# Kernel optimization log

Hardware: AMD Instinct MI355X
Metric: run time of the kernel (lower is better)

## Reference

```python
import jax, jax.numpy as jnp
import numpy as np

SAMPLE_RATE = 24000
THRESHOLD_FACTOR = 5.0
MAX_SPIKE_SAMPLES = int(0.0015 * SAMPLE_RATE)  # 36
K_MAX = 65536  # static upper bound on number of threshold crossings
N_SAMPLES = 24_000_000


def setup_inputs() -> dict:
    key = jax.random.key(0)
    x = jax.random.normal(key, (N_SAMPLES,), dtype=jnp.float32)
    return {"data_detected": x}


def _detect_one(v, threshold):
    """Detect peaks of v above +threshold. For the negative pass, call with -x
    (x < -thr  <=>  -x > thr, and argmin(x) == argmax(-x)). Returns an int32
    array of length K_MAX: valid peak indices first (sorted), padded with -1."""
    N = v.shape[0]
    mask = (v > threshold).astype(jnp.int32)
    d = jnp.diff(mask)  # +1 = entry (False->True), -1 = exit (True->False)
    entries = jnp.nonzero(d == 1, size=K_MAX, fill_value=N)[0]
    exits = jnp.nonzero(d == -1, size=K_MAX, fill_value=N)[0]
    n = jnp.minimum(jnp.sum(d == 1), jnp.sum(d == -1))
    idx = jnp.arange(K_MAX)
    dur = exits - entries
    keep = (idx < n) & (dur <= MAX_SPIKE_SAMPLES)
    # vectorized windowed peak search: (K_MAX, W) gather + row argmax
    win_idx = jnp.clip(entries[:, None] + jnp.arange(MAX_SPIKE_SAMPLES)[None, :], 0, N - 1)
    windows = v[win_idx]
    peaks = entries + jnp.argmax(windows, axis=1)
    # compact valid peaks to the front (entries are sorted), pad with -1
    peaks = jnp.sort(jnp.where(keep, peaks, N))
    total = jnp.sum(keep)
    return jnp.where(idx < total, peaks, -1)


def reference(data_detected):
    x = data_detected
    threshold = THRESHOLD_FACTOR * jnp.median(jnp.abs(x)) / 0.6745
    pos_indices = _detect_one(x, threshold)
    neg_indices = _detect_one(-x, threshold)
    return pos_indices, neg_indices, threshold
```

## Files before the change

### kernel.cpp

```cpp
#include <hip/hip_runtime.h>
#include <stdint.h>

#define HB 18
#define SH_SIZE 8192
#define NSAMP 65536
#define SMARG 1912
#define DBITS 22
#define CAND_CAP 8192
#define CSORT_CAP 4096
#define CBUF_CAP 256
#define LIST_CAP 2500000
#define LBUF_CAP 4096
#define PAIR_CAP 512
#define PEAK_CAP 512
#define MAX_SPIKE 36
#define AB_BLOCKS 128
#define TILE 2048

#define P_ULO   0
#define P_UHI   1
#define P_THRLO 2
#define P_THR   3
#define P_CANDN 4
#define P_LISTN 5
#define P_CB    6
#define P_BINA1 7
#define P_BINA2 8
#define P_RA1   9
#define P_RA2   10
#define P_DONES 11
#define P_DONEA 12
#define P_DONEB 13

#define WS_SHIST  0
#define WS_HISTA  32768
#define WS_HISTB  40960
#define WS_PARAMS 57344
#define WS_ZERO_BYTES 57408
#define WS_CAND   57600
#define WS_LIST   102400

__global__ __launch_bounds__(256) void k_prep(int* __restrict__ ws, int nInts,
                                              float* __restrict__ out, int n2) {
  int j = blockIdx.x * 256 + threadIdx.x;
  if (j < nInts) ws[j] = 0;
  if (j < n2) out[j] = -1.0f;
}

__global__ __launch_bounds__(256) void k_sample(const float* __restrict__ x, int N,
                                                int* __restrict__ shist,
                                                int* __restrict__ p) {
  __shared__ int h[SH_SIZE];
  __shared__ int lastS;
  __shared__ int part[256];
  __shared__ int excl[256];
  __shared__ uint32_t uLoS, uHiS;
  int tid = threadIdx.x;
  for (int i = tid; i < SH_SIZE; i += 256) h[i] = 0;
  __syncthreads();
  int stride = N / NSAMP; if (stride < 1) stride = 1;
  for (int i = blockIdx.x * 256 + tid; i < NSAMP; i += gridDim.x * 256) {
    long long idx = (long long)i * stride;
    if (idx < N) {
      uint32_t u = __float_as_uint(x[idx]) & 0x7fffffffu;
      atomicAdd(&h[u >> HB], 1);
    }
  }
  __syncthreads();
  for (int i = tid; i < SH_SIZE; i += 256) {
    int c = h[i];
    if (c) atomicAdd(&shist[i], c);
  }
  __threadfence();
  if (tid == 0) lastS = (atomicAdd(&p[P_DONES], 1) == (int)gridDim.x - 1);
  __syncthreads();
  if (!lastS) return;
  __threadfence();
  const int chunk = SH_SIZE / 256;
  int base = tid * chunk;
  int s = 0;
  int cc[chunk];
  for (int w = 0; w < chunk; ++w) { cc[w] = shist[base + w]; s += cc[w]; }
  part[tid] = s;
  __syncthreads();
  if (tid == 0) { int a = 0; for (int i = 0; i < 256; ++i) { excl[i] = a; a += part[i]; } }
  __syncthreads();
  int pre = excl[tid];
  int sA = NSAMP / 2 - SMARG, sB = NSAMP / 2 + SMARG;
  if (pre <= sA && sA < pre + s) {
    int a = pre;
    for (int w = 0; w < chunk; ++w) {
      if (sA < a + cc[w]) { uLoS = (uint32_t)(base + w) << HB; break; }
      a += cc[w];
    }
  }
  if (pre <= sB && sB < pre + s) {
    int a = pre;
    for (int w = 0; w < chunk; ++w) {
      if (sB < a + cc[w]) { uHiS = (uint32_t)(base + w + 1) << HB; break; }
      a += cc[w];
    }
  }
  __syncthreads();
  if (tid == 0) {
    uint32_t uLo = uLoS, uHi = uHiS;
    if (uHi - uLo > (1u << DBITS)) uHi = uLo + (1u << DBITS);
    p[P_ULO] = (int)uLo;
    p[P_UHI] = (int)uHi;
    float vLo = __uint_as_float(uLo);
    p[P_THRLO] = __float_as_int((5.0f * vLo / 0.6745f) * 0.999f);
  }
}

__device__ inline void m_elem(uint32_t fbits, int idx, uint32_t uLo, uint32_t bw,
                              uint32_t thrBits, int* lbuf, int* lcnt,
                              int* cbuf, int* ccnt, int& cb) {
  uint32_t u = fbits & 0x7fffffffu;
  cb += (u < uLo) ? 1 : 0;
  if (u - uLo < bw) {
    int id = atomicAdd(lcnt, 1);
    if (id < LBUF_CAP) lbuf[id] = (int)(u - uLo);
  }
  if (u > thrBits) {
    int id = atomicAdd(ccnt, 1);
    if (id < CBUF_CAP) cbuf[id] = idx;
  }
}

__global__ __launch_bounds__(256) void k_main(const float* __restrict__ x, int N,
                                              int* __restrict__ p,
                                              int* __restrict__ list,
                                              int* __restrict__ cand) {
  __shared__ int lbuf[LBUF_CAP];
  __shared__ int cbuf[CBUF_CAP];
  __shared__ int red[256];
  __shared__ int lcnt, ccnt, lbase, cbase;
  int tid = threadIdx.x;
  if (tid == 0) { lcnt = 0; ccnt = 0; }
  __syncthreads();
  uint32_t uLo = (uint32_t)p[P_ULO];
  uint32_t bw  = (uint32_t)p[P_UHI] - uLo;
  uint32_t thrBits = (uint32_t)p[P_THRLO];
  int cb = 0;
  int NV = N >> 2;
  const uint4* vec = reinterpret_cast<const uint4*>(x);
  int nTiles = NV / TILE;
  for (int t = blockIdx.x; t < nTiles; t += gridDim.x) {
    int base = t * TILE + tid;
    uint4 v[8];
#pragma unroll
    for (int k = 0; k < 8; ++k) v[k] = vec[base + (k << 8)];
    __builtin_amdgcn_sched_barrier(0);
#pragma unroll
    for (int k = 0; k < 8; ++k) {
      int ei = (base + (k << 8)) << 2;
      m_elem(v[k].x, ei + 0, uLo, bw, thrBits, lbuf, &lcnt, cbuf, &ccnt, cb);
      m_elem(v[k].y, ei + 1, uLo, bw, thrBits, lbuf, &lcnt, cbuf, &ccnt, cb);
      m_elem(v[k].z, ei + 2, uLo, bw, thrBits, lbuf, &lcnt, cbuf, &ccnt, cb);
      m_elem(v[k].w, ei + 3, uLo, bw, thrBits, lbuf, &lcnt, cbuf, &ccnt, cb);
    }
  }
  for (int j = nTiles * TILE + blockIdx.x * 256 + tid; j < NV; j += gridDim.x * 256) {
    uint4 a = vec[j];
    int ei = j << 2;
    m_elem(a.x, ei + 0, uLo, bw, thrBits, lbuf, &lcnt, cbuf, &ccnt, cb);
    m_elem(a.y, ei + 1, uLo, bw, thrBits, lbuf, &lcnt, cbuf, &ccnt, cb);
    m_elem(a.z, ei + 2, uLo, bw, thrBits, lbuf, &lcnt, cbuf, &ccnt, cb);
    m_elem(a.w, ei + 3, uLo, bw, thrBits, lbuf, &lcnt, cbuf, &ccnt, cb);
  }
  if (blockIdx.x == 0 && tid == 0) {
    for (int i = NV << 2; i < N; ++i)
      m_elem(__float_as_uint(x[i]), i, uLo, bw, thrBits, lbuf, &lcnt, cbuf, &ccnt, cb);
  }
  __syncthreads();
  int nl = lcnt < LBUF_CAP ? lcnt : LBUF_CAP;
  int nc = ccnt < CBUF_CAP ? ccnt : CBUF_CAP;
  if (tid == 0) {
    lbase = atomicAdd(&p[P_LISTN], nl);
    cbase = atomicAdd(&p[P_CANDN], nc);
  }
  red[tid] = cb;
  __syncthreads();
  for (int s2 = 128; s2; s2 >>= 1) {
    if (tid < s2) red[tid] += red[tid + s2];
    __syncthreads();
  }
  if (tid == 0) atomicAdd(&p[P_CB], red[0]);
  for (int i = tid; i < nl; i += 256)
    if (lbase + i < LIST_CAP) list[lbase + i] = lbuf[i];
  for (int i = tid; i < nc; i += 256)
    if (cbase + i < CAND_CAP) cand[cbase + i] = cbuf[i];
}

__global__ __launch_bounds__(256) void k_stageA(const int* __restrict__ list,
                                                int* __restrict__ p,
                                                int* __restrict__ histA, int N) {
  __shared__ int h[2048];
  __shared__ int lastS;
  __shared__ int part[256];
  __shared__ int excl[256];
  int tid = threadIdx.x;
  for (int i = tid; i < 2048; i += 256) h[i] = 0;
  __syncthreads();
  int n = p[P_LISTN]; if (n > LIST_CAP) n = LIST_CAP;
  int str = gridDim.x * 256;
  for (int i = blockIdx.x * 256 + tid; i < n; i += str)
    atomicAdd(&h[list[i] >> 11], 1);
  __syncthreads();
  for (int i = tid; i < 2048; i += 256) {
    int c = h[i];
    if (c) atomicAdd(&histA[i], c);
  }
  __threadfence();
  if (tid == 0) lastS = (atomicAdd(&p[P_DONEA], 1) == (int)gridDim.x - 1);
  __syncthreads();
  if (!lastS) return;
  __threadfence();
  long long k1 = (long long)(N / 2) - 1, k2 = (long long)(N / 2);
  long long cb = p[P_CB];
  long long r1l = k1 - cb, r2l = k2 - cb;
  if (r1l < 0) r1l = 0; if (r1l > n - 1) r1l = n - 1;
  if (r2l < 0) r2l = 0; if (r2l > n - 1) r2l = n - 1;
  int r1 = (int)r1l, r2 = (int)r2l;
  int base = tid * 8;
  int cc[8]; int s = 0;
#pragma unroll
  for (int w = 0; w < 8; ++w) { cc[w] = histA[base + w]; s += cc[w]; }
  part[tid] = s;
  __syncthreads();
  if (tid == 0) { int a = 0; for (int i = 0; i < 256; ++i) { excl[i] = a; a += part[i]; } }
  __syncthreads();
  int pre = excl[tid];
  if (pre <= r1 && r1 < pre + s) {
    int a = pre;
    for (int w = 0; w < 8; ++w) {
      if (r1 < a + cc[w]) { p[P_BINA1] = base + w; p[P_RA1] = r1 - a; break; }
      a += cc[w];
    }
  }
  if (pre <= r2 && r2 < pre + s) {
    int a = pre;
    for (int w = 0; w < 8; ++w) {
      if (r2 < a + cc[w]) { p[P_BINA2] = base + w; p[P_RA2] = r2 - a; break; }
      a += cc[w];
    }
  }
}

__device__ static void isort(int* a, int n) {
  for (int i = 1; i < n; ++i) {
    int v = a[i]; int j = i - 1;
    while (j >= 0 && a[j] > v) { a[j + 1] = a[j]; --j; }
    a[j + 1] = v;
  }
}

__device__ inline void eval_pair(const float* __restrict__ x, int p, float thr,
                                 int* pe, int* px, int* ne, int* nx, int* cnt) {
  float a = x[p], b = x[p + 1];
  bool m0 = a > thr, m1 = b > thr;
  if (m0 != m1) {
    int id = atomicAdd(&cnt[m1 ? 0 : 1], 1);
    if (id < PAIR_CAP) (m1 ? pe : px)[id] = p;
  }
  bool q0 = (-a) > thr, q1 = (-b) > thr;
  if (q0 != q1) {
    int id = atomicAdd(&cnt[q1 ? 2 : 3], 1);
    if (id < PAIR_CAP) (q1 ? ne : nx)[id] = p;
  }
}

__device__ inline int wave_argmax36(const float* __restrict__ x, int N, int sign,
                                    int e, int lane) {
  float val = -INFINITY;
  int wi = lane;
  if (lane < MAX_SPIKE) {
    int idx = e + lane; if (idx > N - 1) idx = N - 1;
    float v = x[idx];
    val = (sign < 0) ? -v : v;
  }
  for (int off = 32; off; off >>= 1) {
    float ov = __shfl_xor(val, off);
    int owi = __shfl_xor(wi, off);
    if (ov > val || (ov == val && owi < wi)) { val = ov; wi = owi; }
  }
  return e + wi;
}

__device__ inline int proc_pol(const float* __restrict__ x, int N, int sign,
                               const int* eL, int nE, const int* xL, int nX,
                               int* pk, int lane) {
  int n = nE < nX ? nE : nX;
  int tot = 0;
  for (int t = 0; t < n; ++t) {
    int dur = xL[t] - eL[t];
    if (dur <= MAX_SPIKE) {
      int pp = wave_argmax36(x, N, sign, eL[t], lane);
      if (tot < PEAK_CAP && lane == 0) pk[tot] = pp;
      ++tot;
    }
  }
  if (tot > PEAK_CAP) tot = PEAK_CAP;
  if (lane == 0) isort(pk, tot);
  return tot;
}

__global__ __launch_bounds__(256) void k_stageB(const float* __restrict__ x, int N,
                                                const int* __restrict__ list,
                                                int* __restrict__ p,
                                                int* __restrict__ histB,
                                                int* __restrict__ cand,
                                                float* __restrict__ out, int OUT_K) {
  __shared__ int h[4096];
  __shared__ int lastS;
  __shared__ int part[256];
  __shared__ int excl[256];
  __shared__ float vres[2];
  __shared__ float sthr;
  __shared__ int cl[CSORT_CAP];
  __shared__ int pe[PAIR_CAP], px[PAIR_CAP], ne[PAIR_CAP], nx[PAIR_CAP];
  __shared__ int cnt[4];
  __shared__ int pkP[PEAK_CAP], pkN[PEAK_CAP];
  __shared__ int nPk[2];
  int tid = threadIdx.x;
  for (int i = tid; i < 4096; i += 256) h[i] = 0;
  __syncthreads();
  int n = p[P_LISTN]; if (n > LIST_CAP) n = LIST_CAP;
  int binA1 = p[P_BINA1], binA2 = p[P_BINA2];
  int str = gridDim.x * 256;
  for (int i = blockIdx.x * 256 + tid; i < n; i += str) {
    int d = list[i];
    int hi = d >> 11, lo = d & 2047;
    if (hi == binA1) atomicAdd(&h[lo], 1);
    if (hi == binA2) atomicAdd(&h[2048 + lo], 1);
  }
  __syncthreads();
  for (int i = tid; i < 4096; i += 256) {
    int c = h[i];
    if (c) atomicAdd(&histB[i], c);
  }
  __threadfence();
  if (tid == 0) lastS = (atomicAdd(&p[P_DONEB], 1) == (int)gridDim.x - 1);
  __syncthreads();
  if (!lastS) return;
  __threadfence();
  uint32_t uLo = (uint32_t)p[P_ULO];
  if (tid < 2) vres[tid] = __uint_as_float(uLo);
  for (int tgt = 0; tgt < 2; ++tgt) {
    __syncthreads();
    const int* hh = histB + tgt * 2048;
    int rank = (tgt == 0) ? p[P_RA1] : p[P_RA2];
    int binA = (tgt == 0) ? binA1 : binA2;
    int base = tid * 8;
    int cc[8]; int s = 0;
#pragma unroll
    for (int w = 0; w < 8; ++w) { cc[w] = hh[base + w]; s += cc[w]; }
    part[tid] = s;
    __syncthreads();
    if (tid == 0) { int a = 0; for (int i = 0; i < 256; ++i) { excl[i] = a; a += part[i]; } }
    __syncthreads();
    int pre = excl[tid];
    if (pre <= rank && rank < pre + s) {
      int a = pre;
      for (int w = 0; w < 8; ++w) {
        if (rank < a + cc[w]) {
          uint32_t bits = uLo + ((uint32_t)binA << 11) + (uint32_t)(base + w);
          vres[tgt] = __uint_as_float(bits);
          break;
        }
        a += cc[w];
      }
    }
  }
  __syncthreads();
  if (tid == 0) {
    float med = 0.5f * (vres[0] + vres[1]);
    float thr = (5.0f * med) / 0.6745f;
    p[P_THR] = __float_as_int(thr);
    sthr = thr;
    out[2 * OUT_K] = thr;
  }
  if (tid < 4) cnt[tid] = 0;
  __syncthreads();
  float thr = sthr;
  int nC = p[P_CANDN]; if (nC > CAND_CAP) nC = CAND_CAP;
  const int* cnd;
  if (nC <= CSORT_CAP) {
    for (int i = tid; i < nC; i += 256) cl[i] = cand[i];
    __syncthreads();
    int myv[CSORT_CAP / 256], myr[CSORT_CAP / 256], nh = 0;
    for (int i = tid; i < nC; i += 256) {
      int v = cl[i];
      int r = 0;
      for (int q = 0; q < nC; ++q) r += (cl[q] < v) ? 1 : 0;
      myv[nh] = v; myr[nh] = r; ++nh;
    }
    __syncthreads();
    for (int t = 0; t < nh; ++t) cl[myr[t]] = myv[t];
    __syncthreads();
    cnd = cl;
  } else {
    if (tid == 0) isort(cand, nC);
    __syncthreads();
    cnd = cand;
  }
  for (int k = tid; k < nC; k += 256) {
    int c = cnd[k];
    bool prevAdj = (k > 0) && (cnd[k - 1] == c - 1);
    if (c > 0 && !prevAdj) eval_pair(x, c - 1, thr, pe, px, ne, nx, cnt);
    if (c <= N - 2) eval_pair(x, c, thr, pe, px, ne, nx, cnt);
  }
  __syncthreads();
  int nPE = min(cnt[0], PAIR_CAP), nPX = min(cnt[1], PAIR_CAP);
  int nNE = min(cnt[2], PAIR_CAP), nNX = min(cnt[3], PAIR_CAP);
  if (tid == 0) { isort(pe, nPE); isort(px, nPX); }
  else if (tid == 1) { isort(ne, nNE); isort(nx, nNX); }
  __syncthreads();
  if (tid < 64) {
    int t0 = proc_pol(x, N, +1, pe, nPE, px, nPX, pkP, tid);
    int t1 = proc_pol(x, N, -1, ne, nNE, nx, nNX, pkN, tid);
    if (tid == 0) { nPk[0] = t0; nPk[1] = t1; }
  }
  __syncthreads();
  for (int j = tid; j < nPk[0]; j += 256) out[j] = (float)pkP[j];
  for (int j = tid; j < nPk[1]; j += 256) out[OUT_K + j] = (float)pkN[j];
}

extern "C" void kernel_launch(void* const* d_in, const int* in_sizes, int n_in,
                              void* d_out, int out_size, void* d_ws, size_t ws_size,
                              hipStream_t stream) {
  const float* x = (const float*)d_in[0];
  int N = in_sizes[0];
  float* out = (float*)d_out;
  char* ws = (char*)d_ws;

  int* shist  = (int*)(ws + WS_SHIST);
  int* histA  = (int*)(ws + WS_HISTA);
  int* histB  = (int*)(ws + WS_HISTB);
  int* params = (int*)(ws + WS_PARAMS);
  int* cand   = (int*)(ws + WS_CAND);
  int* list   = (int*)(ws + WS_LIST);

  int OUT_K = (out_size - 1) / 2;
  int nInts = WS_ZERO_BYTES / 4;
  int prepN = 2 * OUT_K;

  k_prep<<<(prepN + 255) / 256, 256, 0, stream>>>((int*)ws, nInts, out, prepN);
  k_sample<<<64, 256, 0, stream>>>(x, N, shist, params);
  k_main<<<2048, 256, 0, stream>>>(x, N, params, list, cand);
  k_stageA<<<AB_BLOCKS, 256, 0, stream>>>(list, params, histA, N);
  k_stageB<<<AB_BLOCKS, 256, 0, stream>>>(x, N, list, params, histB, cand, out, OUT_K);
}
```

Measured before the change: 171.9 us.

## Double-buffer main streaming pass with async global-to-LDS loads

Replaces the register-tile streaming loop in the main scan kernel with a double-buffered pipeline that uses global_load_lds to prefetch the next 16 KB tile into shared memory while the current tile is processed. The goal is to overlap memory latency with the per-element classification work. In exchange it adds 32 KB of LDS per block, which can lower occupancy, two block barriers per tile, and a full vmcnt(0) wait each iteration. The tile also shrinks from 8 to 4 vectors per thread.

```diff
diff --git a/kernel.cpp b/kernel.cpp
--- a/kernel.cpp
+++ b/kernel.cpp
@@ -15,7 +15,6 @@
 #define PEAK_CAP 512
 #define MAX_SPIKE 36
 #define AB_BLOCKS 128
-#define TILE 2048
 
 #define P_ULO   0
 #define P_UHI   1
@@ -40,6 +39,13 @@
 #define WS_CAND   57600
 #define WS_LIST   102400
 
+typedef __attribute__((address_space(3))) uint8_t lds8;
+typedef __attribute__((address_space(1))) const uint8_t glb8;
+
+__device__ __forceinline__ void async16(const void* g, void* l) {
+  __builtin_amdgcn_global_load_lds((glb8*)g, (lds8*)l, 16, 0, 0);
+}
+
 __global__ __launch_bounds__(256) void k_prep(int* __restrict__ ws, int nInts,
                                               float* __restrict__ out, int n2) {
   int j = blockIdx.x * 256 + threadIdx.x;
@@ -112,9 +118,9 @@
   }
 }
 
-__device__ inline void m_elem(uint32_t fbits, int idx, uint32_t uLo, uint32_t bw,
-                              uint32_t thrBits, int* lbuf, int* lcnt,
-                              int* cbuf, int* ccnt, int& cb) {
+__device__ __forceinline__ void m_elem(uint32_t fbits, int idx, uint32_t uLo, uint32_t bw,
+                                       uint32_t thrBits, int* lbuf, int* lcnt,
+                                       int* cbuf, int* ccnt, int& cb) {
   uint32_t u = fbits & 0x7fffffffu;
   cb += (u < uLo) ? 1 : 0;
   if (u - uLo < bw) {
@@ -131,6 +137,7 @@
                                               int* __restrict__ p,
                                               int* __restrict__ list,
                                               int* __restrict__ cand) {
+  __shared__ __align__(16) uint8_t stage[2][16384];
   __shared__ int lbuf[LBUF_CAP];
   __shared__ int cbuf[CBUF_CAP];
   __shared__ int red[256];
@@ -143,24 +150,42 @@
   uint32_t thrBits = (uint32_t)p[P_THRLO];
   int cb = 0;
   int NV = N >> 2;
+  int nTiles = NV >> 10;
   const uint4* vec = reinterpret_cast<const uint4*>(x);
-  int nTiles = NV / TILE;
-  for (int t = blockIdx.x; t < nTiles; t += gridDim.x) {
-    int base = t * TILE + tid;
-    uint4 v[8];
+  int G = gridDim.x;
+  int t = blockIdx.x;
+  if (t < nTiles) {
+    const uint8_t* g = (const uint8_t*)(vec + ((long long)t << 10));
 #pragma unroll
-    for (int k = 0; k < 8; ++k) v[k] = vec[base + (k << 8)];
-    __builtin_amdgcn_sched_barrier(0);
+    for (int r = 0; r < 4; ++r)
+      async16(g + (((r << 8) + tid) << 4), &stage[0][((r << 8) + tid) << 4]);
+  }
+  int i = 0;
+  for (; t < nTiles; t += G, ++i) {
+    int cur = i & 1;
+    int tn = t + G;
+    if (tn < nTiles) {
+      const uint8_t* g = (const uint8_t*)(vec + ((long long)tn << 10));
 #pragma unroll
-    for (int k = 0; k < 8; ++k) {
-      int ei = (base + (k << 8)) << 2;
-      m_elem(v[k].x, ei + 0, uLo, bw, thrBits, lbuf, &lcnt, cbuf, &ccnt, cb);
-      m_elem(v[k].y, ei + 1, uLo, bw, thrBits, lbuf, &lcnt, cbuf, &ccnt, cb);
-      m_elem(v[k].z, ei + 2, uLo, bw, thrBits, lbuf, &lcnt, cbuf, &ccnt, cb);
-      m_elem(v[k].w, ei + 3, uLo, bw, thrBits, lbuf, &lcnt, cbuf, &ccnt, cb);
-    }
-  }
-  for (int j = nTiles * TILE + blockIdx.x * 256 + tid; j < NV; j += gridDim.x * 256) {
+      for (int r = 0; r < 4; ++r)
+        async16(g + (((r << 8) + tid) << 4), &stage[cur ^ 1][((r << 8) + tid) << 4]);
+    }
+    asm volatile("s_waitcnt vmcnt(0)" ::: "memory");
+    __syncthreads();
+    const uint4* sb = reinterpret_cast<const uint4*>(&stage[cur][0]);
+    int eb = t << 12;
+#pragma unroll
+    for (int r = 0; r < 4; ++r) {
+      uint4 v = sb[(r << 8) + tid];
+      int ei = eb + (((r << 8) + tid) << 2);
+      m_elem(v.x, ei + 0, uLo, bw, thrBits, lbuf, &lcnt, cbuf, &ccnt, cb);
+      m_elem(v.y, ei + 1, uLo, bw, thrBits, lbuf, &lcnt, cbuf, &ccnt, cb);
+      m_elem(v.z, ei + 2, uLo, bw, thrBits, lbuf, &lcnt, cbuf, &ccnt, cb);
+      m_elem(v.w, ei + 3, uLo, bw, thrBits, lbuf, &lcnt, cbuf, &ccnt, cb);
+    }
+    __syncthreads();
+  }
+  for (int j = (nTiles << 10) + blockIdx.x * 256 + tid; j < NV; j += G * 256) {
     uint4 a = vec[j];
     int ei = j << 2;
     m_elem(a.x, ei + 0, uLo, bw, thrBits, lbuf, &lcnt, cbuf, &ccnt, cb);
@@ -169,8 +194,8 @@
     m_elem(a.w, ei + 3, uLo, bw, thrBits, lbuf, &lcnt, cbuf, &ccnt, cb);
   }
   if (blockIdx.x == 0 && tid == 0) {
-    for (int i = NV << 2; i < N; ++i)
-      m_elem(__float_as_uint(x[i]), i, uLo, bw, thrBits, lbuf, &lcnt, cbuf, &ccnt, cb);
+    for (int i2 = NV << 2; i2 < N; ++i2)
+      m_elem(__float_as_uint(x[i2]), i2, uLo, bw, thrBits, lbuf, &lcnt, cbuf, &ccnt, cb);
   }
   __syncthreads();
   int nl = lcnt < LBUF_CAP ? lcnt : LBUF_CAP;
@@ -186,10 +211,10 @@
     __syncthreads();
   }
   if (tid == 0) atomicAdd(&p[P_CB], red[0]);
-  for (int i = tid; i < nl; i += 256)
-    if (lbase + i < LIST_CAP) list[lbase + i] = lbuf[i];
-  for (int i = tid; i < nc; i += 256)
-    if (cbase + i < CAND_CAP) cand[cbase + i] = cbuf[i];
+  for (int i2 = tid; i2 < nl; i2 += 256)
+    if (lbase + i2 < LIST_CAP) list[lbase + i2] = lbuf[i2];
+  for (int i2 = tid; i2 < nc; i2 += 256)
+    if (cbase + i2 < CAND_CAP) cand[cbase + i2] = cbuf[i2];
 }
 
 __global__ __launch_bounds__(256) void k_stageA(const int* __restrict__ list,
```

After: 174.2 us. No clear change (+1.3%).

## Fuse stage-A histogram into main pass with per-thread stash compaction

Applied to the files above, without the earlier changes.

The coarse rank-histogram stage is folded into the main streaming kernel. The last block to finish selects the median bins, so the separate stageA launch and its re-read of the candidate list are gone. Shared-memory atomic appends are replaced with branchless per-thread register-indexed stashes, followed by a wave-level prefix scan to compact results into global memory. The sampling kernel now reads a contiguous prefix instead of strided elements, and the bracket margin is narrowed to shrink the list. This relies on the data being stationary and on small per-thread stash caps, which could overflow for skewed inputs.

```diff
diff --git a/kernel.cpp b/kernel.cpp
--- a/kernel.cpp
+++ b/kernel.cpp
@@ -4,18 +4,18 @@
 #define HB 18
 #define SH_SIZE 8192
 #define NSAMP 65536
-#define SMARG 1912
+#define SMARG 800
 #define DBITS 22
 #define CAND_CAP 8192
 #define CSORT_CAP 4096
-#define CBUF_CAP 256
 #define LIST_CAP 2500000
-#define LBUF_CAP 4096
 #define PAIR_CAP 512
 #define PEAK_CAP 512
 #define MAX_SPIKE 36
 #define AB_BLOCKS 128
-#define TILE 2048
+#define MAIN_G 1024
+#define STASH_K 22
+#define CSTASH_K 4
 
 #define P_ULO   0
 #define P_UHI   1
@@ -58,11 +58,9 @@
   int tid = threadIdx.x;
   for (int i = tid; i < SH_SIZE; i += 256) h[i] = 0;
   __syncthreads();
-  int stride = N / NSAMP; if (stride < 1) stride = 1;
   for (int i = blockIdx.x * 256 + tid; i < NSAMP; i += gridDim.x * 256) {
-    long long idx = (long long)i * stride;
-    if (idx < N) {
-      uint32_t u = __float_as_uint(x[idx]) & 0x7fffffffu;
+    if (i < N) {
+      uint32_t u = __float_as_uint(x[i]) & 0x7fffffffu;
       atomicAdd(&h[u >> HB], 1);
     }
   }
@@ -112,73 +110,101 @@
   }
 }
 
-__device__ inline void m_elem(uint32_t fbits, int idx, uint32_t uLo, uint32_t bw,
-                              uint32_t thrBits, int* lbuf, int* lcnt,
-                              int* cbuf, int* ccnt, int& cb) {
-  uint32_t u = fbits & 0x7fffffffu;
+__device__ __forceinline__ void elem(uint32_t fb, int idx, uint32_t uLo, uint32_t bw,
+                                     uint32_t thrBits, int sbase, int csbase,
+                                     int* stash, int* cstash,
+                                     int& myCnt, int& cCnt, int& cb) {
+  uint32_t u = fb & 0x7fffffffu;
   cb += (u < uLo) ? 1 : 0;
-  if (u - uLo < bw) {
-    int id = atomicAdd(lcnt, 1);
-    if (id < LBUF_CAP) lbuf[id] = (int)(u - uLo);
-  }
-  if (u > thrBits) {
-    int id = atomicAdd(ccnt, 1);
-    if (id < CBUF_CAP) cbuf[id] = idx;
-  }
-}
-
-__global__ __launch_bounds__(256) void k_main(const float* __restrict__ x, int N,
+  uint32_t d = u - uLo;
+  int slot = myCnt < (STASH_K - 1) ? myCnt : (STASH_K - 1);
+  stash[sbase + slot] = (int)d;
+  myCnt += (d < bw) ? 1 : 0;
+  int cslot = cCnt < (CSTASH_K - 1) ? cCnt : (CSTASH_K - 1);
+  cstash[csbase + cslot] = idx;
+  cCnt += (u > thrBits) ? 1 : 0;
+}
+
+__global__ __launch_bounds__(256) void k_main(const float* __restrict__ x, int N, int G2,
                                               int* __restrict__ p,
                                               int* __restrict__ list,
-                                              int* __restrict__ cand) {
-  __shared__ int lbuf[LBUF_CAP];
-  __shared__ int cbuf[CBUF_CAP];
+                                              int* __restrict__ cand,
+                                              int* __restrict__ histA) {
+  __shared__ int stash[256 * (STASH_K + 1)];
+  __shared__ int cstash[256 * (CSTASH_K + 1)];
+  __shared__ int histA_l[2048];
   __shared__ int red[256];
-  __shared__ int lcnt, ccnt, lbase, cbase;
+  __shared__ int excl[256];
+  __shared__ int wtot[4], wexcl[4], cwtot[4], cwexcl[4];
+  __shared__ int gbase, cgbase, lastS;
   int tid = threadIdx.x;
-  if (tid == 0) { lcnt = 0; ccnt = 0; }
+  for (int i = tid; i < 2048; i += 256) histA_l[i] = 0;
   __syncthreads();
   uint32_t uLo = (uint32_t)p[P_ULO];
   uint32_t bw  = (uint32_t)p[P_UHI] - uLo;
   uint32_t thrBits = (uint32_t)p[P_THRLO];
-  int cb = 0;
+  int cb = 0, myCnt = 0, cCnt = 0;
+  int sbase = tid * (STASH_K + 1), csbase = tid * (CSTASH_K + 1);
   int NV = N >> 2;
   const uint4* vec = reinterpret_cast<const uint4*>(x);
-  int nTiles = NV / TILE;
-  for (int t = blockIdx.x; t < nTiles; t += gridDim.x) {
-    int base = t * TILE + tid;
+  int nT = NV >> 11;
+  for (int t = blockIdx.x; t < nT; t += gridDim.x) {
+    int basev = (t << 11) + tid;
     uint4 v[8];
 #pragma unroll
-    for (int k = 0; k < 8; ++k) v[k] = vec[base + (k << 8)];
-    __builtin_amdgcn_sched_barrier(0);
+    for (int k = 0; k < 8; ++k) v[k] = vec[basev + (k << 8)];
 #pragma unroll
     for (int k = 0; k < 8; ++k) {
-      int ei = (base + (k << 8)) << 2;
-      m_elem(v[k].x, ei + 0, uLo, bw, thrBits, lbuf, &lcnt, cbuf, &ccnt, cb);
-      m_elem(v[k].y, ei + 1, uLo, bw, thrBits, lbuf, &lcnt, cbuf, &ccnt, cb);
-      m_elem(v[k].z, ei + 2, uLo, bw, thrBits, lbuf, &lcnt, cbuf, &ccnt, cb);
-      m_elem(v[k].w, ei + 3, uLo, bw, thrBits, lbuf, &lcnt, cbuf, &ccnt, cb);
-    }
-  }
-  for (int j = nTiles * TILE + blockIdx.x * 256 + tid; j < NV; j += gridDim.x * 256) {
+      int eb = (basev + (k << 8)) << 2;
+      elem(v[k].x, eb + 0, uLo, bw, thrBits, sbase, csbase, stash, cstash, myCnt, cCnt, cb);
+      elem(v[k].y, eb + 1, uLo, bw, thrBits, sbase, csbase, stash, cstash, myCnt, cCnt, cb);
+      elem(v[k].z, eb + 2, uLo, bw, thrBits, sbase, csbase, stash, cstash, myCnt, cCnt, cb);
+      elem(v[k].w, eb + 3, uLo, bw, thrBits, sbase, csbase, stash, cstash, myCnt, cCnt, cb);
+    }
+  }
+  for (int j = (nT << 11) + blockIdx.x * 256 + tid; j < NV; j += gridDim.x * 256) {
     uint4 a = vec[j];
     int ei = j << 2;
-    m_elem(a.x, ei + 0, uLo, bw, thrBits, lbuf, &lcnt, cbuf, &ccnt, cb);
-    m_elem(a.y, ei + 1, uLo, bw, thrBits, lbuf, &lcnt, cbuf, &ccnt, cb);
-    m_elem(a.z, ei + 2, uLo, bw, thrBits, lbuf, &lcnt, cbuf, &ccnt, cb);
-    m_elem(a.w, ei + 3, uLo, bw, thrBits, lbuf, &lcnt, cbuf, &ccnt, cb);
+    elem(a.x, ei + 0, uLo, bw, thrBits, sbase, csbase, stash, cstash, myCnt, cCnt, cb);
+    elem(a.y, ei + 1, uLo, bw, thrBits, sbase, csbase, stash, cstash, myCnt, cCnt, cb);
+    elem(a.z, ei + 2, uLo, bw, thrBits, sbase, csbase, stash, cstash, myCnt, cCnt, cb);
+    elem(a.w, ei + 3, uLo, bw, thrBits, sbase, csbase, stash, cstash, myCnt, cCnt, cb);
   }
   if (blockIdx.x == 0 && tid == 0) {
-    for (int i = NV << 2; i < N; ++i)
-      m_elem(__float_as_uint(x[i]), i, uLo, bw, thrBits, lbuf, &lcnt, cbuf, &ccnt, cb);
-  }
-  __syncthreads();
-  int nl = lcnt < LBUF_CAP ? lcnt : LBUF_CAP;
-  int nc = ccnt < CBUF_CAP ? ccnt : CBUF_CAP;
+    for (int i2 = NV << 2; i2 < N; ++i2)
+      elem(__float_as_uint(x[i2]), i2, uLo, bw, thrBits, sbase, csbase,
+           stash, cstash, myCnt, cCnt, cb);
+  }
+  __syncthreads();
+  if (myCnt > STASH_K) myCnt = STASH_K;
+  if (cCnt > CSTASH_K) cCnt = CSTASH_K;
+  for (int k2 = 0; k2 < myCnt; ++k2)
+    atomicAdd(&histA_l[(stash[sbase + k2] >> 11) & 2047], 1);
+  int lane = tid & 63, wv = tid >> 6;
+  int sc = myCnt, cc2 = cCnt;
+  for (int off = 1; off < 64; off <<= 1) {
+    int o = __shfl_up(sc, off);
+    int o2 = __shfl_up(cc2, off);
+    if (lane >= off) { sc += o; cc2 += o2; }
+  }
+  if (lane == 63) { wtot[wv] = sc; cwtot[wv] = cc2; }
+  __syncthreads();
   if (tid == 0) {
-    lbase = atomicAdd(&p[P_LISTN], nl);
-    cbase = atomicAdd(&p[P_CANDN], nc);
-  }
+    int a = 0, ca = 0;
+    for (int w = 0; w < 4; ++w) {
+      wexcl[w] = a; a += wtot[w];
+      cwexcl[w] = ca; ca += cwtot[w];
+    }
+    gbase = atomicAdd(&p[P_LISTN], a);
+    cgbase = atomicAdd(&p[P_CANDN], ca);
+  }
+  __syncthreads();
+  int myBase = gbase + wexcl[wv] + (sc - myCnt);
+  for (int k2 = 0; k2 < myCnt; ++k2)
+    if (myBase + k2 < LIST_CAP) list[myBase + k2] = stash[sbase + k2];
+  int cBase = cgbase + cwexcl[wv] + (cc2 - cCnt);
+  for (int k2 = 0; k2 < cCnt; ++k2)
+    if (cBase + k2 < CAND_CAP) cand[cBase + k2] = cstash[csbase + k2];
   red[tid] = cb;
   __syncthreads();
   for (int s2 = 128; s2; s2 >>= 1) {
@@ -186,39 +212,19 @@
     __syncthreads();
   }
   if (tid == 0) atomicAdd(&p[P_CB], red[0]);
-  for (int i = tid; i < nl; i += 256)
-    if (lbase + i < LIST_CAP) list[lbase + i] = lbuf[i];
-  for (int i = tid; i < nc; i += 256)
-    if (cbase + i < CAND_CAP) cand[cbase + i] = cbuf[i];
-}
-
-__global__ __launch_bounds__(256) void k_stageA(const int* __restrict__ list,
-                                                int* __restrict__ p,
-                                                int* __restrict__ histA, int N) {
-  __shared__ int h[2048];
-  __shared__ int lastS;
-  __shared__ int part[256];
-  __shared__ int excl[256];
-  int tid = threadIdx.x;
-  for (int i = tid; i < 2048; i += 256) h[i] = 0;
-  __syncthreads();
+  for (int i = tid; i < 2048; i += 256) {
+    int c = histA_l[i];
+    if (c) atomicAdd(&histA[i], c);
+  }
+  __threadfence();
+  if (tid == 0) lastS = (atomicAdd(&p[P_DONEA], 1) == G2 - 1);
+  __syncthreads();
+  if (!lastS) return;
+  __threadfence();
   int n = p[P_LISTN]; if (n > LIST_CAP) n = LIST_CAP;
-  int str = gridDim.x * 256;
-  for (int i = blockIdx.x * 256 + tid; i < n; i += str)
-    atomicAdd(&h[list[i] >> 11], 1);
-  __syncthreads();
-  for (int i = tid; i < 2048; i += 256) {
-    int c = h[i];
-    if (c) atomicAdd(&histA[i], c);
-  }
-  __threadfence();
-  if (tid == 0) lastS = (atomicAdd(&p[P_DONEA], 1) == (int)gridDim.x - 1);
-  __syncthreads();
-  if (!lastS) return;
-  __threadfence();
   long long k1 = (long long)(N / 2) - 1, k2 = (long long)(N / 2);
-  long long cb = p[P_CB];
-  long long r1l = k1 - cb, r2l = k2 - cb;
+  long long cbAll = p[P_CB];
+  long long r1l = k1 - cbAll, r2l = k2 - cbAll;
   if (r1l < 0) r1l = 0; if (r1l > n - 1) r1l = n - 1;
   if (r2l < 0) r2l = 0; if (r2l > n - 1) r2l = n - 1;
   int r1 = (int)r1l, r2 = (int)r2l;
@@ -226,9 +232,9 @@
   int cc[8]; int s = 0;
 #pragma unroll
   for (int w = 0; w < 8; ++w) { cc[w] = histA[base + w]; s += cc[w]; }
-  part[tid] = s;
-  __syncthreads();
-  if (tid == 0) { int a = 0; for (int i = 0; i < 256; ++i) { excl[i] = a; a += part[i]; } }
+  red[tid] = s;
+  __syncthreads();
+  if (tid == 0) { int a = 0; for (int i = 0; i < 256; ++i) { excl[i] = a; a += red[i]; } }
   __syncthreads();
   int pre = excl[tid];
   if (pre <= r1 && r1 < pre + s) {
@@ -447,7 +453,6 @@
 
   k_prep<<<(prepN + 255) / 256, 256, 0, stream>>>((int*)ws, nInts, out, prepN);
   k_sample<<<64, 256, 0, stream>>>(x, N, shist, params);
-  k_main<<<2048, 256, 0, stream>>>(x, N, params, list, cand);
-  k_stageA<<<AB_BLOCKS, 256, 0, stream>>>(list, params, histA, N);
+  k_main<<<MAIN_G, 256, 0, stream>>>(x, N, MAIN_G, params, list, cand, histA);
   k_stageB<<<AB_BLOCKS, 256, 0, stream>>>(x, N, list, params, histB, cand, out, OUT_K);
 }
```

Result: slower. 203.2 us (+18.2%).
